# Kernel optimization log

Hardware: AMD Instinct MI355X
Metric: run time of the kernel (lower is better)

## Reference

```python
import jax, jax.numpy as jnp
import numpy as np

D_MODEL = 1024
N_HEAD = 16
D_K = D_MODEL // N_HEAD


def setup_inputs() -> dict:
    key = jax.random.key(0)
    ks = jax.random.split(key, 11)
    B, S = 2, 2048
    scale = 1.0 / np.sqrt(D_MODEL)
    inp = {
        "q": jax.random.normal(ks[0], (B, S, D_MODEL), jnp.float32),
        "k": jax.random.normal(ks[1], (B, S, D_MODEL), jnp.float32),
        "v": jax.random.normal(ks[2], (B, S, D_MODEL), jnp.float32),
        "Wq": jax.random.normal(ks[3], (D_MODEL, D_MODEL), jnp.float32) * scale,
        "bq": jnp.zeros((D_MODEL,), jnp.float32),
        "Wk": jax.random.normal(ks[4], (D_MODEL, D_MODEL), jnp.float32) * scale,
        "bk": jnp.zeros((D_MODEL,), jnp.float32),
        "Wv": jax.random.normal(ks[5], (D_MODEL, D_MODEL), jnp.float32) * scale,
        "bv": jnp.zeros((D_MODEL,), jnp.float32),
        "Wo": jax.random.normal(ks[6], (D_MODEL, D_MODEL), jnp.float32) * scale,
        "bo": jnp.zeros((D_MODEL,), jnp.float32),
    }
    return inp


def reference(q, k, v, Wq, bq, Wk, bk, Wv, bv, Wo, bo):
    B, S, _ = q.shape
    # QKV projections, split heads: [B, H, S, d_k]
    def proj(x, W, b):
        y = x @ W + b  # [B, S, D]
        return y.reshape(B, -1, N_HEAD, D_K).transpose(0, 2, 1, 3)

    qh = proj(q, Wq, bq)
    kh = proj(k, Wk, bk)
    vh = proj(v, Wv, bv)

    # sigmoid attention (no row normalization)
    scores = jnp.einsum("bhsd,bhtd->bhst", qh, kh) / jnp.sqrt(jnp.float32(D_K))
    attn = jax.nn.sigmoid(scores)  # [B, H, S, S]
    ctx = jnp.einsum("bhst,bhtd->bhsd", attn, vh)

    # merge heads and output projection
    ctx = ctx.transpose(0, 2, 1, 3).reshape(B, S, D_MODEL)
    return ctx @ Wo + bo
```

## Files before the change

### kernel.cpp

```cpp
#include <hip/hip_runtime.h>
#include <stdint.h>

typedef _Float16 f16;
typedef _Float16 f16x4 __attribute__((ext_vector_type(4)));
typedef _Float16 f16x8 __attribute__((ext_vector_type(8)));
typedef float f32x4 __attribute__((ext_vector_type(4)));
typedef float f32x16 __attribute__((ext_vector_type(16)));
typedef unsigned int u32;

#define D_MODEL 1024
#define N_HEAD 16
#define BATCH 2
#define SEQ 2048
#define MTOT 4096
#define NQKV 3072

__device__ __forceinline__ void llds16(const void* g, void* l) {
  __builtin_amdgcn_global_load_lds(
      (const __attribute__((address_space(1))) unsigned int*)g,
      (__attribute__((address_space(3))) unsigned int*)l, 16, 0, 0);
}

__device__ __forceinline__ float fast_rcp(float x) {
#if __has_builtin(__builtin_amdgcn_rcpf)
  return __builtin_amdgcn_rcpf(x);
#else
  return 1.0f / x;
#endif
}

#define SIG(x) fast_rcp(1.0f + __expf((x) * -0.125f))

__device__ __forceinline__ u32 pk2(float a, float b) {
  auto h = __builtin_amdgcn_cvt_pkrtz(a, b);
  return __builtin_bit_cast(u32, h);
}

__global__ void k_cvt3(const float* __restrict__ q, const float* __restrict__ k,
                       const float* __restrict__ v, f16* __restrict__ dst) {
  const int idx = (blockIdx.x * 256 + threadIdx.x) * 8;
  const int seg = idx >> 22;
  const int off = idx & ((1 << 22) - 1);
  const float* s = (seg == 0) ? q : (seg == 1) ? k : v;
  const float4 a = *(const float4*)(s + off);
  const float4 b = *(const float4*)(s + off + 4);
  f16x8 o;
  o[0] = (f16)a.x; o[1] = (f16)a.y; o[2] = (f16)a.z; o[3] = (f16)a.w;
  o[4] = (f16)b.x; o[5] = (f16)b.y; o[6] = (f16)b.z; o[7] = (f16)b.w;
  *(f16x8*)(dst + idx) = o;
}

__global__ void k_tw(const float* __restrict__ Wq, const float* __restrict__ Wk,
                     const float* __restrict__ Wv, const float* __restrict__ Wo,
                     f16* __restrict__ WqkvT, f16* __restrict__ WoT) {
  __shared__ float t[32][33];
  const int z = blockIdx.z;
  const float* W = (z == 0) ? Wq : (z == 1) ? Wk : (z == 2) ? Wv : Wo;
  f16* dst = (z < 3) ? (WqkvT + (size_t)z * 1024 * 1024) : WoT;
  const int bx = blockIdx.x * 32, by = blockIdx.y * 32;
  const int tx = threadIdx.x, ty = threadIdx.y;
#pragma unroll
  for (int i = 0; i < 32; i += 8)
    t[ty + i][tx] = W[(size_t)(by + ty + i) * 1024 + bx + tx];
  __syncthreads();
#pragma unroll
  for (int i = 0; i < 32; i += 8)
    dst[(size_t)(bx + ty + i) * 1024 + by + tx] = (f16)t[tx][ty + i];
}

template <int Nd, int MODE>
__global__ __launch_bounds__(512, 4) void k_gemm(const f16* __restrict__ A0,
                                                 const f16* __restrict__ A1,
                                                 const f16* __restrict__ A2,
                                                 const f16* __restrict__ BT,
                                                 const float* __restrict__ b0,
                                                 const float* __restrict__ b1,
                                                 const float* __restrict__ b2,
                                                 void* __restrict__ Cout,
                                                 f16* __restrict__ Vt) {
  constexpr int Kd = 1024;
  constexpr int NBX = Nd / 128;
  constexpr int NWG = (MTOT / 128) * NBX;
  __shared__ __align__(16) f16 As[2][8192];
  __shared__ __align__(16) f16 Bs[2][8192];
  int id = blockIdx.x;
  id = (id & 7) * (NWG / 8) + (id >> 3);
  const int n0 = (id % NBX) * 128, m0 = (id / NBX) * 128;
  const f16* A = (Nd == 1024) ? A0 : (n0 < 1024 ? A0 : n0 < 2048 ? A1 : A2);
  const int tid = threadIdx.x, w = tid >> 6, ln = tid & 63;
  const int wm = w >> 2, wn = w & 3;
  f32x4 acc[4][2] = {};

  auto stage = [&](int buf, int kt) {
    const int k0 = kt * 64;
#pragma unroll
    for (int i = 0; i < 2; ++i) {
      const int c = w * 2 + i;
      const int r = c * 8 + (ln >> 3);
      const int g = ln & 7;
      const int ko = k0 + ((g ^ (r & 7)) * 8);
      llds16(A + (size_t)(m0 + r) * Kd + ko, &As[buf][c * 512]);
      llds16(BT + (size_t)(n0 + r) * Kd + ko, &Bs[buf][c * 512]);
    }
  };
  stage(0, 0);
  __syncthreads();
  int cur = 0;
  for (int kt = 0; kt < Kd / 64; ++kt) {
    if (kt < Kd / 64 - 1) stage(cur ^ 1, kt + 1);
#pragma unroll
    for (int kk = 0; kk < 2; ++kk) {
      f16x8 af[4], bf[2];
#pragma unroll
      for (int mi = 0; mi < 4; ++mi) {
        const int r = wm * 64 + mi * 16 + (ln & 15);
        const int g = kk * 4 + (ln >> 4);
        af[mi] = *(const f16x8*)(&As[cur][r * 64 + ((g ^ (r & 7)) * 8)]);
      }
#pragma unroll
      for (int nf = 0; nf < 2; ++nf) {
        const int r = wn * 32 + nf * 16 + (ln & 15);
        const int g = kk * 4 + (ln >> 4);
        bf[nf] = *(const f16x8*)(&Bs[cur][r * 64 + ((g ^ (r & 7)) * 8)]);
      }
#pragma unroll
      for (int mi = 0; mi < 4; ++mi)
#pragma unroll
        for (int nf = 0; nf < 2; ++nf)
          acc[mi][nf] = __builtin_amdgcn_mfma_f32_16x16x32_f16(af[mi], bf[nf], acc[mi][nf], 0, 0, 0);
    }
    __syncthreads();
    cur ^= 1;
  }
  const float* bb = (Nd == 1024) ? b0 : (n0 < 1024 ? b0 : n0 < 2048 ? b1 : b2);
  const int nb = n0 & 1023;
  if (MODE == 0 && n0 >= 2048) {
#pragma unroll
    for (int mi = 0; mi < 4; ++mi)
#pragma unroll
      for (int nf = 0; nf < 2; ++nf) {
        const int cl = wn * 32 + nf * 16 + (ln & 15);
        const int colg = n0 - 2048 + cl;
        const int hd = colg >> 6, d = colg & 63;
        const int row0 = m0 + wm * 64 + mi * 16 + (ln >> 4) * 4;
        const int bI = row0 >> 11, s = row0 & 2047;
        const float bias = bb[nb + cl];
        f16x4 pv;
#pragma unroll
        for (int r = 0; r < 4; ++r) pv[r] = (f16)(acc[mi][nf][r] + bias);
        *(f16x4*)(&Vt[((size_t)(bI * 16 + hd) * 64 + d) * SEQ + s]) = pv;
      }
  } else {
#pragma unroll
    for (int mi = 0; mi < 4; ++mi)
#pragma unroll
      for (int nf = 0; nf < 2; ++nf)
#pragma unroll
        for (int r = 0; r < 4; ++r) {
          const int row = m0 + wm * 64 + mi * 16 + (ln >> 4) * 4 + r;
          const int cl = wn * 32 + nf * 16 + (ln & 15);
          const float val = acc[mi][nf][r] + bb[nb + cl];
          if (MODE == 1)
            ((float*)Cout)[(size_t)row * Nd + n0 + cl] = val;
          else
            ((f16*)Cout)[(size_t)row * Nd + n0 + cl] = (f16)val;
        }
  }
}

__global__ __launch_bounds__(256, 2) void k_attn(const f16* __restrict__ QKV,
                                                 const f16* __restrict__ Vt,
                                                 f16* __restrict__ ctx) {
  __shared__ __align__(16) f16 Ks[2][4096];
  __shared__ __align__(16) f16 Vs[2][4096];
  int id = blockIdx.x;
  id = (id & 7) * 64 + (id >> 3);
  const int qt = id & 15, hd = (id >> 4) & 15, b = id >> 8;
  const int tid = threadIdx.x, w = tid >> 6, ln = tid & 63;
  const int lh = ln >> 5, l31 = ln & 31;
  const int q0 = qt * 128 + w * 32;
  const f16* Qb = QKV + ((size_t)b * SEQ) * NQKV + hd * 64;
  const f16* Kb = QKV + ((size_t)b * SEQ) * NQKV + 1024 + hd * 64;
  const f16* Vtb = Vt + (size_t)(b * N_HEAD + hd) * 64 * SEQ;

  f16x8 aq[4];
#pragma unroll
  for (int kk = 0; kk < 4; ++kk)
    aq[kk] = *(const f16x8*)(Qb + (size_t)(q0 + l31) * NQKV + kk * 16 + lh * 8);

  f32x16 oacc0 = {}, oacc1 = {};

  auto stage = [&](int buf, int kt) {
    const int kv0 = kt * 64;
#pragma unroll
    for (int i = 0; i < 2; ++i) {
      const int c = w * 2 + i;
      const int r = c * 8 + (ln >> 3);
      const int g = ln & 7;
      llds16(Kb + (size_t)(kv0 + r) * NQKV + ((g ^ (r & 7)) * 8), &Ks[buf][c * 512]);
      llds16(Vtb + (size_t)r * SEQ + kv0 + ((g ^ (r & 7)) * 8), &Vs[buf][c * 512]);
    }
  };
  stage(0, 0);
  __syncthreads();
  int cur = 0;
  for (int kt = 0; kt < SEQ / 64; ++kt) {
    if (kt < SEQ / 64 - 1) stage(cur ^ 1, kt + 1);
    f32x16 sacc0 = {}, sacc1 = {};
#pragma unroll
    for (int kk = 0; kk < 4; ++kk) {
      {
        const int r = l31;
        const f16x8 ak = *(const f16x8*)(&Ks[cur][r * 64 + (((kk * 2 + lh) ^ (r & 7)) * 8)]);
        sacc0 = __builtin_amdgcn_mfma_f32_32x32x16_f16(ak, aq[kk], sacc0, 0, 0, 0);
      }
      {
        const int r = 32 + l31;
        const f16x8 ak = *(const f16x8*)(&Ks[cur][r * 64 + (((kk * 2 + lh) ^ (r & 7)) * 8)]);
        sacc1 = __builtin_amdgcn_mfma_f32_32x32x16_f16(ak, aq[kk], sacc1, 0, 0, 0);
      }
    }
    f16x8 pa[4];
#pragma unroll
    for (int kvt = 0; kvt < 2; ++kvt) {
      const f32x16 sc = kvt ? sacc1 : sacc0;
#pragma unroll
      for (int hf = 0; hf < 2; ++hf) {
        const int b8 = hf * 8;
        u32 X = pk2(SIG(sc[b8 + 0]), SIG(sc[b8 + 1]));
        u32 Y = pk2(SIG(sc[b8 + 2]), SIG(sc[b8 + 3]));
        u32 Z = pk2(SIG(sc[b8 + 4]), SIG(sc[b8 + 5]));
        u32 W = pk2(SIG(sc[b8 + 6]), SIG(sc[b8 + 7]));
        asm volatile("v_permlane32_swap_b32 %0, %1" : "+v"(X), "+v"(Z));
        asm volatile("v_permlane32_swap_b32 %0, %1" : "+v"(Y), "+v"(W));
        union { u32 uw[4]; f16x8 v; } u;
        u.uw[0] = X; u.uw[1] = Y; u.uw[2] = Z; u.uw[3] = W;
        pa[kvt * 2 + hf] = u.v;
      }
    }
#pragma unroll
    for (int c = 0; c < 4; ++c) {
      {
        const int d = l31;
        const f16x8 bv = *(const f16x8*)(&Vs[cur][d * 64 + (((c * 2 + lh) ^ (d & 7)) * 8)]);
        oacc0 = __builtin_amdgcn_mfma_f32_32x32x16_f16(pa[c], bv, oacc0, 0, 0, 0);
      }
      {
        const int d = 32 + l31;
        const f16x8 bv = *(const f16x8*)(&Vs[cur][d * 64 + (((c * 2 + lh) ^ (d & 7)) * 8)]);
        oacc1 = __builtin_amdgcn_mfma_f32_32x32x16_f16(pa[c], bv, oacc1, 0, 0, 0);
      }
    }
    __syncthreads();
    cur ^= 1;
  }
#pragma unroll
  for (int dt = 0; dt < 2; ++dt) {
    const int dcol = hd * 64 + dt * 32 + l31;
#pragma unroll
    for (int r = 0; r < 16; ++r) {
      const int ql = (r & 3) + 8 * (r >> 2) + 4 * lh;
      const float v = dt ? oacc1[r] : oacc0[r];
      ctx[((size_t)b * SEQ + q0 + ql) * D_MODEL + dcol] = (f16)v;
    }
  }
}

extern "C" void kernel_launch(void* const* d_in, const int* in_sizes, int n_in,
                              void* d_out, int out_size, void* d_ws, size_t ws_size,
                              hipStream_t stream) {
  (void)in_sizes; (void)n_in; (void)out_size; (void)ws_size;
  const float* q  = (const float*)d_in[0];
  const float* k  = (const float*)d_in[1];
  const float* v  = (const float*)d_in[2];
  const float* Wq = (const float*)d_in[3];
  const float* bq = (const float*)d_in[4];
  const float* Wk = (const float*)d_in[5];
  const float* bk = (const float*)d_in[6];
  const float* Wv = (const float*)d_in[7];
  const float* bv = (const float*)d_in[8];
  const float* Wo = (const float*)d_in[9];
  const float* bo = (const float*)d_in[10];
  float* out = (float*)d_out;

  char* p = (char*)d_ws;
  const size_t SZ_X = (size_t)MTOT * D_MODEL * sizeof(f16);
  f16* qb    = (f16*)p; p += 3 * SZ_X;
  f16* WqkvT = (f16*)p; p += 3 * (size_t)1024 * 1024 * sizeof(f16);
  f16* WoT   = (f16*)p; p += (size_t)1024 * 1024 * sizeof(f16);
  f16* QKVb  = (f16*)p; p += (size_t)MTOT * NQKV * sizeof(f16);
  f16* Vtb   = (f16*)p; p += SZ_X;
  f16* ctx   = (f16*)p; p += SZ_X;
  f16* kb = qb + (size_t)MTOT * D_MODEL;
  f16* vb = kb + (size_t)MTOT * D_MODEL;

  k_cvt3<<<3 * MTOT * D_MODEL / 2048, 256, 0, stream>>>(q, k, v, qb);
  k_tw<<<dim3(32, 32, 4), dim3(32, 8), 0, stream>>>(Wq, Wk, Wv, Wo, WqkvT, WoT);
  k_gemm<NQKV, 0><<<(MTOT / 128) * (NQKV / 128), 512, 0, stream>>>(
      qb, kb, vb, WqkvT, bq, bk, bv, QKVb, Vtb);
  k_attn<<<(SEQ / 128) * N_HEAD * BATCH, 256, 0, stream>>>(QKVb, Vtb, ctx);
  k_gemm<1024, 1><<<(MTOT / 128) * (1024 / 128), 512, 0, stream>>>(
      ctx, ctx, ctx, WoT, bo, bo, bo, out, nullptr);
}
```

Measured before the change: 233.9 us.

## Split attention over two KV halves and fold softmax scale into Q

Attention blocks now each process half of the key/value sequence, doubling the grid, and write fp16 partial outputs that a new elementwise kernel sums before the output projection. The Q projection epilogue pre-multiplies by the score scale times log2(e), so the sigmoid uses a raw exp2. This raises parallelism and CU fill for attention, at the cost of extra partial-output memory traffic, an extra launch, and fp16 rounding of partials.

Result: no change. 234.3 us (+0.2%).

```diff
diff --git a/kernel.cpp b/kernel.cpp
--- a/kernel.cpp
+++ b/kernel.cpp
@@ -1,5 +1,6 @@
 #include <hip/hip_runtime.h>
 #include <stdint.h>
+#include <math.h>
 
 typedef _Float16 f16;
 typedef _Float16 f16x4 __attribute__((ext_vector_type(4)));
@@ -14,6 +15,7 @@
 #define SEQ 2048
 #define MTOT 4096
 #define NQKV 3072
+#define QSCALE 0.18033688011112042f
 
 __device__ __forceinline__ void llds16(const void* g, void* l) {
   __builtin_amdgcn_global_load_lds(
@@ -29,7 +31,15 @@
 #endif
 }
 
-#define SIG(x) fast_rcp(1.0f + __expf((x) * -0.125f))
+__device__ __forceinline__ float fast_exp2(float x) {
+#if __has_builtin(__builtin_amdgcn_exp2f)
+  return __builtin_amdgcn_exp2f(x);
+#else
+  return exp2f(x);
+#endif
+}
+
+#define SIG(s) fast_rcp(1.0f + fast_exp2(-(s)))
 
 __device__ __forceinline__ u32 pk2(float a, float b) {
   auto h = __builtin_amdgcn_cvt_pkrtz(a, b);
@@ -151,6 +161,7 @@
         *(f16x4*)(&Vt[((size_t)(bI * 16 + hd) * 64 + d) * SEQ + s]) = pv;
       }
   } else {
+    const float sc = (MODE == 0 && n0 < 1024) ? QSCALE : 1.0f;
 #pragma unroll
     for (int mi = 0; mi < 4; ++mi)
 #pragma unroll
@@ -159,7 +170,7 @@
         for (int r = 0; r < 4; ++r) {
           const int row = m0 + wm * 64 + mi * 16 + (ln >> 4) * 4 + r;
           const int cl = wn * 32 + nf * 16 + (ln & 15);
-          const float val = acc[mi][nf][r] + bb[nb + cl];
+          const float val = (acc[mi][nf][r] + bb[nb + cl]) * sc;
           if (MODE == 1)
             ((float*)Cout)[(size_t)row * Nd + n0 + cl] = val;
           else
@@ -170,15 +181,16 @@
 
 __global__ __launch_bounds__(256, 2) void k_attn(const f16* __restrict__ QKV,
                                                  const f16* __restrict__ Vt,
-                                                 f16* __restrict__ ctx) {
+                                                 f16* __restrict__ Opart) {
   __shared__ __align__(16) f16 Ks[2][4096];
   __shared__ __align__(16) f16 Vs[2][4096];
   int id = blockIdx.x;
-  id = (id & 7) * 64 + (id >> 3);
-  const int qt = id & 15, hd = (id >> 4) & 15, b = id >> 8;
+  id = (id & 7) * 128 + (id >> 3);
+  const int qt = id & 15, hd = (id >> 4) & 15, b = (id >> 8) & 1, half = id >> 9;
   const int tid = threadIdx.x, w = tid >> 6, ln = tid & 63;
   const int lh = ln >> 5, l31 = ln & 31;
   const int q0 = qt * 128 + w * 32;
+  const int kvbase = half * (SEQ / 2);
   const f16* Qb = QKV + ((size_t)b * SEQ) * NQKV + hd * 64;
   const f16* Kb = QKV + ((size_t)b * SEQ) * NQKV + 1024 + hd * 64;
   const f16* Vtb = Vt + (size_t)(b * N_HEAD + hd) * 64 * SEQ;
@@ -191,7 +203,7 @@
   f32x16 oacc0 = {}, oacc1 = {};
 
   auto stage = [&](int buf, int kt) {
-    const int kv0 = kt * 64;
+    const int kv0 = kvbase + kt * 64;
 #pragma unroll
     for (int i = 0; i < 2; ++i) {
       const int c = w * 2 + i;
@@ -204,8 +216,8 @@
   stage(0, 0);
   __syncthreads();
   int cur = 0;
-  for (int kt = 0; kt < SEQ / 64; ++kt) {
-    if (kt < SEQ / 64 - 1) stage(cur ^ 1, kt + 1);
+  for (int kt = 0; kt < SEQ / 128; ++kt) {
+    if (kt < SEQ / 128 - 1) stage(cur ^ 1, kt + 1);
     f32x16 sacc0 = {}, sacc1 = {};
 #pragma unroll
     for (int kk = 0; kk < 4; ++kk) {
@@ -254,6 +266,7 @@
     __syncthreads();
     cur ^= 1;
   }
+  f16* ob = Opart + (size_t)half * MTOT * D_MODEL;
 #pragma unroll
   for (int dt = 0; dt < 2; ++dt) {
     const int dcol = hd * 64 + dt * 32 + l31;
@@ -261,9 +274,20 @@
     for (int r = 0; r < 16; ++r) {
       const int ql = (r & 3) + 8 * (r >> 2) + 4 * lh;
       const float v = dt ? oacc1[r] : oacc0[r];
-      ctx[((size_t)b * SEQ + q0 + ql) * D_MODEL + dcol] = (f16)v;
+      ob[((size_t)b * SEQ + q0 + ql) * D_MODEL + dcol] = (f16)v;
     }
   }
+}
+
+__global__ void k_add(const f16* __restrict__ a, const f16* __restrict__ b,
+                      f16* __restrict__ o) {
+  const int i = (blockIdx.x * 256 + threadIdx.x) * 8;
+  const f16x8 x = *(const f16x8*)(a + i);
+  const f16x8 y = *(const f16x8*)(b + i);
+  f16x8 r;
+#pragma unroll
+  for (int j = 0; j < 8; ++j) r[j] = (f16)((float)x[j] + (float)y[j]);
+  *(f16x8*)(o + i) = r;
 }
 
 extern "C" void kernel_launch(void* const* d_in, const int* in_sizes, int n_in,
@@ -290,6 +314,7 @@
   f16* WoT   = (f16*)p; p += (size_t)1024 * 1024 * sizeof(f16);
   f16* QKVb  = (f16*)p; p += (size_t)MTOT * NQKV * sizeof(f16);
   f16* Vtb   = (f16*)p; p += SZ_X;
+  f16* Opart = (f16*)p; p += 2 * SZ_X;
   f16* ctx   = (f16*)p; p += SZ_X;
   f16* kb = qb + (size_t)MTOT * D_MODEL;
   f16* vb = kb + (size_t)MTOT * D_MODEL;
@@ -298,7 +323,9 @@
   k_tw<<<dim3(32, 32, 4), dim3(32, 8), 0, stream>>>(Wq, Wk, Wv, Wo, WqkvT, WoT);
   k_gemm<NQKV, 0><<<(MTOT / 128) * (NQKV / 128), 512, 0, stream>>>(
       qb, kb, vb, WqkvT, bq, bk, bv, QKVb, Vtb);
-  k_attn<<<(SEQ / 128) * N_HEAD * BATCH, 256, 0, stream>>>(QKVb, Vtb, ctx);
+  k_attn<<<(SEQ / 128) * N_HEAD * BATCH * 2, 256, 0, stream>>>(QKVb, Vtb, Opart);
+  k_add<<<MTOT * D_MODEL / 2048, 256, 0, stream>>>(
+      Opart, Opart + (size_t)MTOT * D_MODEL, ctx);
   k_gemm<1024, 1><<<(MTOT / 128) * (1024 / 128), 512, 0, stream>>>(
       ctx, ctx, ctx, WoT, bo, bo, bo, out, nullptr);
 }
```
